# Optimization experiments

Measured on AMD Instinct MI355X. Metric: run time of the kernel, lower is better.

The kernel has to match this reference:

```python
import jax, jax.numpy as jnp
import numpy as np

EPS = 1e-20
K = 3  # kernel_size


def _patches(x, k=K):
    # emulates KernelChannels.kernel_channels / F.unfold with stride=1, padding=0, dilation=1
    # x: (B, C, H, W) -> (B, C, k*k, H-k+1, W-k+1); depth index kk = i*k + j maps to offset (i, j)
    Ho = x.shape[2] - k + 1
    Wo = x.shape[3] - k + 1
    return jnp.stack([x[:, :, i:i + Ho, j:j + Wo] for i in range(k) for j in range(k)], axis=2)


def setup_inputs() -> dict:
    key = jax.random.key(0)
    ks = jax.random.split(key, 13)
    B, C, O, H, W = 2, 32, 32, 256, 512
    Ho, Wo = H - K + 1, W - K + 1
    d = jax.random.uniform(ks[0], (B, C, H, W), dtype=jnp.float32)
    cd = jax.random.uniform(ks[1], (B, C, H, W), dtype=jnp.float32)
    s = jax.random.uniform(ks[2], (B, C, H, W), dtype=jnp.float32)
    cs = jax.random.uniform(ks[3], (B, C, H, W), dtype=jnp.float32)
    gx = jax.random.normal(ks[4], (B, C, H, W), dtype=jnp.float32)
    cgx = jax.random.uniform(ks[5], (B, C, H, W), dtype=jnp.float32)
    gy = jax.random.normal(ks[6], (B, C, H, W), dtype=jnp.float32)
    cgy = jax.random.uniform(ks[7], (B, C, H, W), dtype=jnp.float32)
    s_prod_roll = jax.random.uniform(ks[8], (B, C, K * K, Ho, Wo), dtype=jnp.float32)
    # learned parameters (raw; EnforcePos applies softplus inside forward)
    w_prop = jax.random.normal(ks[9], (1, 1, 1, 1), dtype=jnp.float32) * 0.1
    spatial_weight = jax.random.normal(ks[10], (C, 1, K * K, 1, 1), dtype=jnp.float32) * 0.1
    channel_weight = jax.random.normal(ks[11], (O, C, 1, 1), dtype=jnp.float32) * 0.1
    bias = jax.random.normal(ks[12], (1, O, 1, 1), dtype=jnp.float32) * 0.01
    return {"d": d, "cd": cd, "s": s, "cs": cs, "gx": gx, "cgx": cgx, "gy": gy,
            "cgy": cgy, "s_prod_roll": s_prod_roll, "w_prop": w_prop,
            "spatial_weight": spatial_weight, "channel_weight": channel_weight, "bias": bias}


def reference(d, cd, s, cs, gx, cgx, gy, cgy, s_prod_roll,
              w_prop, spatial_weight, channel_weight, bias):
    stride = 1
    # roll-based vertical neighbor gather with confidence zeroing at borders
    d_up = jnp.roll(d, 1, axis=2)
    cd_up = jnp.roll(cd, 1, axis=2).at[:, :, 0, :].set(0.0)
    s_up = jnp.roll(s, 1, axis=2)
    d_down = jnp.roll(d, -1, axis=2)
    cd_down = jnp.roll(cd, -1, axis=2).at[:, :, -1, :].set(0.0)
    s_down = jnp.roll(s, -1, axis=2)

    cgy_from_ds = s * s_up * s_down * cd_up * cd_up  # faithful to source (cd_up twice)
    height = (cd_up * d_up + cd_down * d_down) / (cd_up + cd_down + EPS)
    gy_from_ds = (d_down - d_up) / 2.0 / (height + EPS)

    w = jax.nn.softplus(w_prop)[0, 0, 0, 0]  # EnforcePos on w_prop
    gy_f = (w * cgy * gy + cgy_from_ds * gy_from_ds) / (w * cgy + cgy_from_ds + EPS)
    cgy_f = (w * cgy + cgy_from_ds) / (w + 1.0)

    # kernel-channel expansion (B, C, k*k, Ho, Wo)
    gy_roll = _patches(gy_f)
    cgy_roll = _patches(cgy_f)
    cgy_prop = cgy_roll * s_prod_roll

    # grouped conv3d with (C,1,k*k,1,1) kernel, groups=C == per-channel weighted sum over k*k
    sw = jax.nn.softplus(spatial_weight)[:, 0, :, 0, 0]  # (C, k*k)
    nom = jnp.einsum('bckhw,ck->bchw', cgy_prop * gy_roll, sw)
    den = jnp.einsum('bckhw,ck->bchw', cgy_prop, sw)
    gy_sp = nom / (den + EPS)
    cgy_sp = den / jnp.sum(sw)

    # 1x1 conv2d across channels (groups=1)
    cw = jax.nn.softplus(channel_weight)[:, :, 0, 0]  # (O, C)
    nom2 = jnp.einsum('bchw,oc->bohw', cgy_sp * gy_sp, cw)
    den2 = jnp.einsum('bchw,oc->bohw', cgy_sp, cw)
    gy_out = nom2 / (den2 + EPS) + bias
    cgy_out = den2 / jnp.sum(cw)
    return (gy_out * stride, cgy_out / stride / stride)
```

## Files before the change

kernel.cpp:

```cpp
#include <hip/hip_runtime.h>

#define EPSF 1e-20f

typedef float v2f __attribute__((ext_vector_type(2)));
typedef float v4f __attribute__((ext_vector_type(4)));

constexpr int B_ = 2, C_ = 32, O_ = 32, H_ = 256, W_ = 512;
constexpr int HO = 254, WO = 510;
constexpr int HW  = H_ * W_;
constexpr int PLO = HO * WO;
constexpr int OUT1 = B_ * O_ * PLO;
constexpr int IMG  = B_ * C_ * HW;
constexpr int WT2  = 128;
constexpr int NB1  = IMG / 4 / 256;

__device__ __forceinline__ float sp_(float x) { return log1pf(expf(x)); }
__device__ __forceinline__ float rcp_(float x) { return __builtin_amdgcn_rcpf(x); }

__device__ __forceinline__ unsigned bfpack(float g, float c) {
  unsigned ug = __float_as_uint(g);
  unsigned uc = __float_as_uint(c);
  ug = ug + 0x7FFFu + ((ug >> 16) & 1u);
  uc = uc + 0x7FFFu + ((uc >> 16) & 1u);
  return (ug >> 16) | (uc & 0xFFFF0000u);
}
__device__ __forceinline__ float bf_lo(unsigned u) { return __uint_as_float(u << 16); }
__device__ __forceinline__ float bf_hi(unsigned u) { return __uint_as_float(u & 0xFFFF0000u); }

__global__ __launch_bounds__(256) void k1_gyf(const float* __restrict__ d,
                                              const float* __restrict__ cd,
                                              const float* __restrict__ s,
                                              const float* __restrict__ gy,
                                              const float* __restrict__ cgy,
                                              const float* __restrict__ w_prop,
                                              const float* __restrict__ spw,
                                              const float* __restrict__ chw,
                                              float* __restrict__ params,
                                              unsigned* __restrict__ I) {
  __shared__ float red[256];
  const int t = threadIdx.x;

  if (blockIdx.x == NB1) {
    float l1 = 0.f;
    for (int i = t; i < 288; i += 256) { float v = sp_(spw[i]); params[16 + i] = v; l1 += v; }
    red[t] = l1; __syncthreads();
    for (int k = 128; k > 0; k >>= 1) { if (t < k) red[t] += red[t + k]; __syncthreads(); }
    float SW = red[0]; __syncthreads();
    float l2 = 0.f;
    for (int i = t; i < 1024; i += 256) {
      int o = i >> 5, c = i & 31;
      float v = sp_(chw[o * C_ + c]);
      params[304 + c * O_ + o] = v;
      l2 += v;
    }
    red[t] = l2; __syncthreads();
    for (int k = 128; k > 0; k >>= 1) { if (t < k) red[t] += red[t + k]; __syncthreads(); }
    if (t == 0) { params[0] = sp_(w_prop[0]); params[1] = SW; params[2] = red[0]; }
    return;
  }

  const float w      = sp_(w_prop[0]);
  const float inv_w1 = rcp_(w + 1.0f);
  const int idx = blockIdx.x * 256 + t;
  const long i4 = (long)idx * 4;
  const int h = (int)((i4 >> 9) & (H_ - 1));
  const long up = (h == 0)      ? i4 + (long)(H_ - 1) * W_ : i4 - W_;
  const long dn = (h == H_ - 1) ? i4 - (long)(H_ - 1) * W_ : i4 + W_;

  float4 duv = *(const float4*)(d + up);
  float4 ddv = *(const float4*)(d + dn);
  float4 sv  = *(const float4*)(s + i4);
  float4 suv = *(const float4*)(s + up);
  float4 sdv = *(const float4*)(s + dn);
  float4 cduv = (h == 0)      ? make_float4(0.f, 0.f, 0.f, 0.f) : *(const float4*)(cd + up);
  float4 cddv = (h == H_ - 1) ? make_float4(0.f, 0.f, 0.f, 0.f) : *(const float4*)(cd + dn);
  float4 gyv  = *(const float4*)(gy + i4);
  float4 cgyv = *(const float4*)(cgy + i4);

  const float* pdu = (const float*)&duv;  const float* pdd = (const float*)&ddv;
  const float* ps  = (const float*)&sv;   const float* psu = (const float*)&suv;
  const float* psd = (const float*)&sdv;  const float* pcu = (const float*)&cduv;
  const float* pcd = (const float*)&cddv; const float* pg  = (const float*)&gyv;
  const float* pc  = (const float*)&cgyv;

  uint4 o;
  unsigned* po = (unsigned*)&o;
#pragma unroll
  for (int j = 0; j < 4; ++j) {
    const float cu = pcu[j], cdn = pcd[j];
    const float cfd = ps[j] * psu[j] * psd[j] * cu * cu;
    const float height = (cu * pdu[j] + cdn * pdd[j]) * rcp_(cu + cdn + EPSF);
    const float gfd = (pdd[j] - pdu[j]) * 0.5f * rcp_(height + EPSF);
    const float a = w * pc[j];
    const float P = (a * pg[j] + cfd * gfd) * inv_w1;
    const float Q = (a + cfd) * inv_w1;
    po[j] = bfpack(P, Q);
  }
  *(uint4*)(I + i4) = o;
}

__global__ __launch_bounds__(512) void k2_fused(const unsigned* __restrict__ I,
                                                const float* __restrict__ spr,
                                                const float* __restrict__ params,
                                                const float* __restrict__ bias,
                                                float* __restrict__ out) {
  __shared__ v2f AB[C_][WT2 + 2];

  const int b   = blockIdx.z;
  const int ho  = blockIdx.y;
  const int wo0 = blockIdx.x * WT2;
  const int t   = threadIdx.x;

  const float invSW = rcp_(params[1]);
  const float invCW = rcp_(params[2]);

  const int pp = t & 63;
  const int cg = __builtin_amdgcn_readfirstlane(t >> 6);
  const int wo  = wo0 + 2 * pp;
  const int wos = (wo <= WO - 2) ? wo : (WO - 2);

#pragma unroll
  for (int ci = 0; ci < 4; ++ci) {
    const int c = cg * 4 + ci;
    const unsigned* Ip = I + (b * C_ + c) * HW + ho * W_ + wos;
    uint2 r0a = *(const uint2*)(Ip);
    uint2 r0b = *(const uint2*)(Ip + 2);
    uint2 r1a = *(const uint2*)(Ip + W_);
    uint2 r1b = *(const uint2*)(Ip + W_ + 2);
    uint2 r2a = *(const uint2*)(Ip + 2 * W_);
    uint2 r2b = *(const uint2*)(Ip + 2 * W_ + 2);

    const float* sp = spr + (long)(b * C_ + c) * 9 * PLO + ho * WO + wos;
    v2f spv[9];
#pragma unroll
    for (int k = 0; k < 9; ++k) spv[k] = *(const v2f*)(sp + (long)k * PLO);

    unsigned urow[3][4] = {{r0a.x, r0a.y, r0b.x, r0b.y},
                           {r1a.x, r1a.y, r1b.x, r1b.y},
                           {r2a.x, r2a.y, r2b.x, r2b.y}};
    float P[3][4], Q[3][4];
#pragma unroll
    for (int i = 0; i < 3; ++i)
#pragma unroll
      for (int j = 0; j < 4; ++j) { P[i][j] = bf_lo(urow[i][j]); Q[i][j] = bf_hi(urow[i][j]); }

    const float* swc = params + 16 + c * 9;
    v2f nom = (v2f){0.f, 0.f};
    v2f den = (v2f){0.f, 0.f};
#pragma unroll
    for (int i = 0; i < 3; ++i) {
#pragma unroll
      for (int j = 0; j < 3; ++j) {
        const v2f tk = spv[i * 3 + j] * swc[i * 3 + j];
        nom += tk * (v2f){P[i][j], P[i][j + 1]};
        den += tk * (v2f){Q[i][j], Q[i][j + 1]};
      }
    }
    *(v4f*)&AB[c][2 * pp] = (v4f){nom.x * invSW, den.x * invSW,
                                  nom.y * invSW, den.y * invSW};
  }
  __syncthreads();

  const int px  = t & 127;
  const int og  = __builtin_amdgcn_readfirstlane(t >> 7);
  const int wob = wo0 + px;

  v2f ab[C_];
#pragma unroll
  for (int c = 0; c < C_; ++c) ab[c] = AB[c][px];

  const float* cwT = params + 304;
  v2f acc[8];
#pragma unroll
  for (int oj = 0; oj < 8; ++oj) acc[oj] = (v2f){0.f, 0.f};
#pragma unroll
  for (int c = 0; c < C_; ++c) {
#pragma unroll
    for (int oj = 0; oj < 8; ++oj)
      acc[oj] += ab[c] * cwT[c * O_ + og * 8 + oj];
  }

  if (wob < WO) {
    const int obase = b * O_ * PLO + ho * WO + wob;
#pragma unroll
    for (int oj = 0; oj < 8; ++oj) {
      const int o = og * 8 + oj;
      out[obase + o * PLO]        = acc[oj].x * rcp_(acc[oj].y + EPSF) + bias[o];
      out[OUT1 + obase + o * PLO] = acc[oj].y * invCW;
    }
  }
}

extern "C" void kernel_launch(void* const* d_in, const int* in_sizes, int n_in,
                              void* d_out, int out_size, void* d_ws, size_t ws_size,
                              hipStream_t stream) {
  const float* d      = (const float*)d_in[0];
  const float* cd     = (const float*)d_in[1];
  const float* s      = (const float*)d_in[2];
  const float* gy     = (const float*)d_in[6];
  const float* cgy    = (const float*)d_in[7];
  const float* spr    = (const float*)d_in[8];
  const float* w_prop = (const float*)d_in[9];
  const float* spw    = (const float*)d_in[10];
  const float* chw    = (const float*)d_in[11];
  const float* bias   = (const float*)d_in[12];
  float* out = (float*)d_out;

  float* params = (float*)d_ws;
  unsigned* I   = (unsigned*)d_ws + 4096;

  k1_gyf<<<NB1 + 1, 256, 0, stream>>>(d, cd, s, gy, cgy, w_prop, spw, chw, params, I);

  dim3 g2(4, HO, B_);
  k2_fused<<<g2, 512, 0, stream>>>(I, spr, params, bias, out);
}
```

Measured before the change: 136.1 us.

## Widen fused-kernel tiles to 256 columns with 4-wide vector loads per thread

The fused spatial and channel kernel now runs 1024-thread blocks over 256-column tiles. Adjacent tiles overlap by two columns, so the last tile needs no bounds masking. Each thread handles 4 output columns per channel using 16-byte loads of the packed intermediate and s_prod_roll, replacing the earlier 8-byte loads. This is meant to improve memory-access efficiency and reduce redundant halo reads, at the cost of a few duplicate output writes and higher per-block resource use.

```diff
diff --git a/kernel.cpp b/kernel.cpp
--- a/kernel.cpp
+++ b/kernel.cpp
@@ -11,11 +11,15 @@
 constexpr int PLO = HO * WO;
 constexpr int OUT1 = B_ * O_ * PLO;
 constexpr int IMG  = B_ * C_ * HW;
-constexpr int WT2  = 128;
+constexpr int WT2  = 256;
 constexpr int NB1  = IMG / 4 / 256;
 
 __device__ __forceinline__ float sp_(float x) { return log1pf(expf(x)); }
 __device__ __forceinline__ float rcp_(float x) { return __builtin_amdgcn_rcpf(x); }
+
+__device__ __forceinline__ uint4 ld_u4(const unsigned* p) { uint4 v; __builtin_memcpy(&v, p, 16); return v; }
+__device__ __forceinline__ uint2 ld_u2(const unsigned* p) { uint2 v; __builtin_memcpy(&v, p, 8);  return v; }
+__device__ __forceinline__ v4f   ld_f4(const float* p)    { v4f  v; __builtin_memcpy(&v, p, 16); return v; }
 
 __device__ __forceinline__ unsigned bfpack(float g, float c) {
   unsigned ug = __float_as_uint(g);
@@ -99,95 +103,87 @@
   *(uint4*)(I + i4) = o;
 }
 
-__global__ __launch_bounds__(512) void k2_fused(const unsigned* __restrict__ I,
-                                                const float* __restrict__ spr,
-                                                const float* __restrict__ params,
-                                                const float* __restrict__ bias,
-                                                float* __restrict__ out) {
-  __shared__ v2f AB[C_][WT2 + 2];
+__global__ __launch_bounds__(1024) void k2_fused(const unsigned* __restrict__ I,
+                                                 const float* __restrict__ spr,
+                                                 const float* __restrict__ params,
+                                                 const float* __restrict__ bias,
+                                                 float* __restrict__ out) {
+  __shared__ v2f AB[C_][WT2];
 
   const int b   = blockIdx.z;
   const int ho  = blockIdx.y;
-  const int wo0 = blockIdx.x * WT2;
+  const int wo0 = blockIdx.x * (WT2 - 2);
   const int t   = threadIdx.x;
 
   const float invSW = rcp_(params[1]);
   const float invCW = rcp_(params[2]);
 
-  const int pp = t & 63;
-  const int cg = __builtin_amdgcn_readfirstlane(t >> 6);
-  const int wo  = wo0 + 2 * pp;
-  const int wos = (wo <= WO - 2) ? wo : (WO - 2);
-
-#pragma unroll
-  for (int ci = 0; ci < 4; ++ci) {
-    const int c = cg * 4 + ci;
-    const unsigned* Ip = I + (b * C_ + c) * HW + ho * W_ + wos;
-    uint2 r0a = *(const uint2*)(Ip);
-    uint2 r0b = *(const uint2*)(Ip + 2);
-    uint2 r1a = *(const uint2*)(Ip + W_);
-    uint2 r1b = *(const uint2*)(Ip + W_ + 2);
-    uint2 r2a = *(const uint2*)(Ip + 2 * W_);
-    uint2 r2b = *(const uint2*)(Ip + 2 * W_ + 2);
-
-    const float* sp = spr + (long)(b * C_ + c) * 9 * PLO + ho * WO + wos;
-    v2f spv[9];
-#pragma unroll
-    for (int k = 0; k < 9; ++k) spv[k] = *(const v2f*)(sp + (long)k * PLO);
-
-    unsigned urow[3][4] = {{r0a.x, r0a.y, r0b.x, r0b.y},
-                           {r1a.x, r1a.y, r1b.x, r1b.y},
-                           {r2a.x, r2a.y, r2b.x, r2b.y}};
-    float P[3][4], Q[3][4];
-#pragma unroll
-    for (int i = 0; i < 3; ++i)
-#pragma unroll
-      for (int j = 0; j < 4; ++j) { P[i][j] = bf_lo(urow[i][j]); Q[i][j] = bf_hi(urow[i][j]); }
+  const int ql = t & 63;
+  const int wv = __builtin_amdgcn_readfirstlane(t >> 6);
+  const int wq = wo0 + 4 * ql;
+
+#pragma unroll
+  for (int it = 0; it < 2; ++it) {
+    const int c = wv * 2 + it;
+    const unsigned* Ip = I + (b * C_ + c) * HW + ho * W_ + wq;
+    const float*    sp = spr + (long)(b * C_ + c) * 9 * PLO + (long)ho * WO + wq;
+
+    uint4 A0 = ld_u4(Ip);            uint2 E0 = ld_u2(Ip + 4);
+    uint4 A1 = ld_u4(Ip + W_);       uint2 E1 = ld_u2(Ip + W_ + 4);
+    uint4 A2 = ld_u4(Ip + 2 * W_);   uint2 E2 = ld_u2(Ip + 2 * W_ + 4);
+    v4f sp4[9];
+#pragma unroll
+    for (int k = 0; k < 9; ++k) sp4[k] = ld_f4(sp + (long)k * PLO);
+
+    float P[3][6], Q[3][6];
+    const unsigned r0[6] = {A0.x, A0.y, A0.z, A0.w, E0.x, E0.y};
+    const unsigned r1[6] = {A1.x, A1.y, A1.z, A1.w, E1.x, E1.y};
+    const unsigned r2[6] = {A2.x, A2.y, A2.z, A2.w, E2.x, E2.y};
+#pragma unroll
+    for (int j = 0; j < 6; ++j) {
+      P[0][j] = bf_lo(r0[j]); Q[0][j] = bf_hi(r0[j]);
+      P[1][j] = bf_lo(r1[j]); Q[1][j] = bf_hi(r1[j]);
+      P[2][j] = bf_lo(r2[j]); Q[2][j] = bf_hi(r2[j]);
+    }
 
     const float* swc = params + 16 + c * 9;
-    v2f nom = (v2f){0.f, 0.f};
-    v2f den = (v2f){0.f, 0.f};
+    v4f nom = (v4f){0.f, 0.f, 0.f, 0.f};
+    v4f den = (v4f){0.f, 0.f, 0.f, 0.f};
 #pragma unroll
     for (int i = 0; i < 3; ++i) {
 #pragma unroll
       for (int j = 0; j < 3; ++j) {
-        const v2f tk = spv[i * 3 + j] * swc[i * 3 + j];
-        nom += tk * (v2f){P[i][j], P[i][j + 1]};
-        den += tk * (v2f){Q[i][j], Q[i][j + 1]};
+        const v4f tk = sp4[i * 3 + j] * swc[i * 3 + j];
+        nom += tk * (v4f){P[i][j], P[i][j + 1], P[i][j + 2], P[i][j + 3]};
+        den += tk * (v4f){Q[i][j], Q[i][j + 1], Q[i][j + 2], Q[i][j + 3]};
       }
     }
-    *(v4f*)&AB[c][2 * pp] = (v4f){nom.x * invSW, den.x * invSW,
-                                  nom.y * invSW, den.y * invSW};
+    *(v4f*)&AB[c][4 * ql]     = (v4f){nom.x * invSW, den.x * invSW, nom.y * invSW, den.y * invSW};
+    *(v4f*)&AB[c][4 * ql + 2] = (v4f){nom.z * invSW, den.z * invSW, nom.w * invSW, den.w * invSW};
   }
   __syncthreads();
 
-  const int px  = t & 127;
-  const int og  = __builtin_amdgcn_readfirstlane(t >> 7);
-  const int wob = wo0 + px;
-
-  v2f ab[C_];
-#pragma unroll
-  for (int c = 0; c < C_; ++c) ab[c] = AB[c][px];
-
+  const int px = t & 255;
+  const int og = __builtin_amdgcn_readfirstlane(t >> 8);
   const float* cwT = params + 304;
+
   v2f acc[8];
 #pragma unroll
   for (int oj = 0; oj < 8; ++oj) acc[oj] = (v2f){0.f, 0.f};
 #pragma unroll
   for (int c = 0; c < C_; ++c) {
+    const v2f ab = AB[c][px];
 #pragma unroll
     for (int oj = 0; oj < 8; ++oj)
-      acc[oj] += ab[c] * cwT[c * O_ + og * 8 + oj];
-  }
-
-  if (wob < WO) {
-    const int obase = b * O_ * PLO + ho * WO + wob;
-#pragma unroll
-    for (int oj = 0; oj < 8; ++oj) {
-      const int o = og * 8 + oj;
-      out[obase + o * PLO]        = acc[oj].x * rcp_(acc[oj].y + EPSF) + bias[o];
-      out[OUT1 + obase + o * PLO] = acc[oj].y * invCW;
-    }
+      acc[oj] += ab * cwT[c * O_ + og * 8 + oj];
+  }
+
+  const long obase = (long)b * O_ * PLO + (long)ho * WO + wo0 + px;
+#pragma unroll
+  for (int oj = 0; oj < 8; ++oj) {
+    const int o = og * 8 + oj;
+    out[obase + (long)o * PLO]        = acc[oj].x * rcp_(acc[oj].y + EPSF) + bias[o];
+    out[OUT1 + obase + (long)o * PLO] = acc[oj].y * invCW;
   }
 }
 
@@ -211,6 +207,6 @@
 
   k1_gyf<<<NB1 + 1, 256, 0, stream>>>(d, cd, s, gy, cgy, w_prop, spw, chw, params, I);
 
-  dim3 g2(4, HO, B_);
-  k2_fused<<<g2, 512, 0, stream>>>(I, spr, params, bias, out);
-}
+  dim3 g2(2, HO, B_);
+  k2_fused<<<g2, 1024, 0, stream>>>(I, spr, params, bias, out);
+}
```

Result: slower. 149.7 us (+10.0%).
